# Optimization experiments

Hardware: AMD Instinct MI355X
Metric: run time of the kernel (lower is better)

Reference implementation:

```python
import jax, jax.numpy as jnp
from jax import lax
import numpy as np

B = 512      # instances
C = 64       # cases (segments)
HID = 1024
ATT = 128


def _conv(x, w, b):
    # torch Conv2d(kernel=5, padding=2), NCHW / OIHW layout
    y = lax.conv_general_dilated(x, w, (1, 1), [(2, 2), (2, 2)],
                                 dimension_numbers=('NCHW', 'OIHW', 'NCHW'))
    return y + b[None, :, None, None]


def _pool(x):
    # MaxPool2d(2)
    return lax.reduce_window(x, -jnp.inf, lax.max, (1, 1, 2, 2), (1, 1, 2, 2), 'VALID')


def setup_inputs() -> dict:
    key = jax.random.key(0)
    ks = jax.random.split(key, 20)

    def rn(k, shape, scale=0.05):
        return jax.random.normal(k, shape, dtype=jnp.float32) * scale

    inp = {
        'data': jax.random.normal(ks[0], (B, 3, 128, 128), dtype=jnp.float32),
        'case_ids': jnp.sort(jax.random.randint(ks[1], (B,), 0, C, dtype=jnp.int32)),
    }
    chans = [(3, 8), (8, 16), (16, 32), (32, 64), (64, 128)]
    for i, (ci, co) in enumerate(chans):
        inp[f'conv_w{i + 1}'] = rn(ks[2 + 2 * i], (co, ci, 5, 5))
        inp[f'conv_b{i + 1}'] = jnp.zeros((co,), jnp.float32)
    inp['fc_w'] = rn(ks[12], (HID, 128 * 4 * 4), 0.02)
    inp['fc_b'] = jnp.zeros((HID,), jnp.float32)
    inp['att_w1'] = rn(ks[13], (ATT, HID), 0.02)
    inp['att_b1'] = jnp.zeros((ATT,), jnp.float32)
    inp['att_w2'] = rn(ks[14], (1, ATT), 0.02)
    inp['att_b2'] = jnp.zeros((1,), jnp.float32)
    inp['clf_w'] = rn(ks[15], (1, HID), 0.02)
    inp['clf_b'] = jnp.zeros((1,), jnp.float32)
    return inp


def reference(data, case_ids, conv_w1, conv_b1, conv_w2, conv_b2, conv_w3, conv_b3,
              conv_w4, conv_b4, conv_w5, conv_b5, fc_w, fc_b,
              att_w1, att_b1, att_w2, att_b2, clf_w, clf_b):
    x = data
    for w, b in ((conv_w1, conv_b1), (conv_w2, conv_b2), (conv_w3, conv_b3),
                 (conv_w4, conv_b4), (conv_w5, conv_b5)):
        x = jax.nn.relu(_pool(_conv(x, w, b)))
    emb = x.reshape(x.shape[0], -1) @ fc_w.T + fc_b          # (B, HID)

    # --- segment (per-case) attention pooling, vectorized over all cases ---
    logits = (jnp.tanh(emb @ att_w1.T + att_b1) @ att_w2.T + att_b2)[:, 0]  # (B,)
    seg_max = jax.ops.segment_max(logits, case_ids, num_segments=C)
    seg_max = jnp.where(jnp.isfinite(seg_max), seg_max, 0.0)  # guard empty segments
    e = jnp.exp(logits - lax.stop_gradient(seg_max)[case_ids])
    denom = jax.ops.segment_sum(e, case_ids, num_segments=C)
    wgt = e / denom[case_ids]                                  # segment softmax
    aggr = jax.ops.segment_sum(wgt[:, None] * emb, case_ids, num_segments=C)  # (C, HID)

    # --- classifier ---
    return jax.nn.sigmoid(aggr @ clf_w.T + clf_b)              # (C, 1)
```

## Files before the change

kernel.cpp:

```cpp
#include <hip/hip_runtime.h>
#include <hip/hip_bf16.h>
#include <math.h>

#define BATCH 512
#define NSEG  64
#define HID   1024
#define ATT   128

typedef __attribute__((ext_vector_type(8))) __bf16 bf16x8;
typedef __attribute__((ext_vector_type(4))) __bf16 bf16x4;
typedef __attribute__((ext_vector_type(4))) float  f32x4;

__device__ inline void wcv(const float* __restrict__ w, __bf16* __restrict__ wt,
                           int t, int Ci, int Co) {
    int j  = t & 7;
    int t2 = t >> 3;
    int co = t2 % Co;
    int k8 = t2 / Co;
    int k  = k8 * 8 + j;
    int tap = k / Ci, ci = k % Ci;
    wt[t] = (__bf16)w[(co * Ci + ci) * 25 + tap];
}

__global__ void wprep_k(const float* __restrict__ cw1, const float* __restrict__ cw2,
                        const float* __restrict__ cw3, const float* __restrict__ cw4,
                        const float* __restrict__ cw5, const float* __restrict__ fcw,
                        __bf16* __restrict__ wt1, __bf16* __restrict__ wt2,
                        __bf16* __restrict__ wt3, __bf16* __restrict__ wt4,
                        __bf16* __restrict__ wt5, __bf16* __restrict__ wfc) {
    int t = blockIdx.x * 256 + threadIdx.x;
    if (t < 2048) {
        int j = t & 7, m = (t >> 3) & 15, k8 = t >> 7;
        int k = k8 * 8 + j, tap = k >> 2, ci = k & 3;
        float v = 0.f;
        if (m < 8 && ci < 3 && tap < 25) v = cw1[(m * 3 + ci) * 25 + tap];
        wt1[t] = (__bf16)v;
        return;
    }
    t -= 2048;
    if (t < 3200)  { wcv(cw2, wt2, t, 8, 16);   return; }
    t -= 3200;
    if (t < 12800) { wcv(cw3, wt3, t, 16, 32);  return; }
    t -= 12800;
    if (t < 51200) { wcv(cw4, wt4, t, 32, 64);  return; }
    t -= 51200;
    if (t < 204800){ wcv(cw5, wt5, t, 64, 128); return; }
    t -= 204800;
    if (t < 2097152) {
        int j = t & 7, t2 = t >> 3, o = t2 & 1023, k8 = t2 >> 10;
        wfc[t] = (__bf16)fcw[(size_t)o * 2048 + k8 * 8 + j];
    }
}

__global__ void watt_k(const float* __restrict__ w, __bf16* __restrict__ wt) {
    int t = blockIdx.x * 256 + threadIdx.x;
    if (t >= 131072) return;
    int j  = t & 7;
    int t2 = t >> 3;
    int o  = t2 & 127;
    int k8 = t2 >> 7;
    wt[t] = (__bf16)w[(size_t)o * 1024 + k8 * 8 + j];
}

__global__ __launch_bounds__(256) void conv1_mfma_k(
    const float* __restrict__ in, const __bf16* __restrict__ Wt,
    const float* __restrict__ bias, __bf16* __restrict__ out) {
    constexpr int W  = 128;
    constexpr int R  = 4;
    constexpr int RP = R + 4;
    constexpr int WP = W + 4;

    __shared__ __align__(16) __bf16 xs[RP * WP * 4];

    const int tid = threadIdx.x;
    const int b   = blockIdx.x >> 5;
    const int y0  = (blockIdx.x & 31) * R;
    const float* inb = in + (size_t)b * 3 * 16384;

    if (tid < RP * 4) {
        int r = tid >> 2, s = tid & 3;
        int c = (s < 2) ? s : (128 + s);
        *(bf16x4*)(xs + (r * WP + c) * 4) = (bf16x4){};
    }
    {
        int r  = tid >> 5;
        int g  = tid & 31;
        int gy = y0 + r - 2;
        int c0 = g * 4;
        bf16x8 lo = {}, hi = {};
        if ((unsigned)gy < 128u) {
            const float* p = inb + (size_t)gy * 128 + c0;
            float4 a = *(const float4*)(p);
            float4 q = *(const float4*)(p + 16384);
            float4 c = *(const float4*)(p + 32768);
            lo[0] = (__bf16)a.x; lo[1] = (__bf16)q.x; lo[2] = (__bf16)c.x;
            lo[4] = (__bf16)a.y; lo[5] = (__bf16)q.y; lo[6] = (__bf16)c.y;
            hi[0] = (__bf16)a.z; hi[1] = (__bf16)q.z; hi[2] = (__bf16)c.z;
            hi[4] = (__bf16)a.w; hi[5] = (__bf16)q.w; hi[6] = (__bf16)c.w;
        }
        *(bf16x8*)(xs + (r * WP + c0 + 2) * 4)     = lo;
        *(bf16x8*)(xs + (r * WP + c0 + 2) * 4 + 8) = hi;
    }
    __syncthreads();

    const int lane = tid & 63, wave = tid >> 6;
    const int quad = lane >> 4, l15 = lane & 15;
    constexpr int F = 8;

    int pbase[F];
    f32x4 acc[F];
#pragma unroll
    for (int f = 0; f < F; ++f) {
        int row = 2 * (wave >> 1) + (f >> 2);
        int col = (wave & 1) * 64 + (f & 3) * 16 + l15;
        pbase[f] = ((row + 2) * WP + col + 2) * 8;
        acc[f] = f32x4{0.f, 0.f, 0.f, 0.f};
    }
    const char* xsb = (const char*)xs;

#pragma unroll
    for (int kt = 0; kt < 4; ++kt) {
        int k8 = kt * 4 + quad;
        int tap0 = k8 * 2, tap1 = tap0 + 1;
        int t0 = tap0 < 25 ? tap0 : 0;
        int t1 = tap1 < 25 ? tap1 : 0;
        int s0 = ((t0 / 5 - 2) * WP + (t0 % 5 - 2)) * 8;
        int s1 = ((t1 / 5 - 2) * WP + (t1 % 5 - 2)) * 8;
        bf16x8 av = *(const bf16x8*)(Wt + ((size_t)k8 * 16 + l15) * 8);
#pragma unroll
        for (int f = 0; f < F; ++f) {
            bf16x4 b0 = *(const bf16x4*)(xsb + pbase[f] + s0);
            bf16x4 b1 = *(const bf16x4*)(xsb + pbase[f] + s1);
            bf16x8 bv = __builtin_shufflevector(b0, b1, 0, 1, 2, 3, 4, 5, 6, 7);
            acc[f] = __builtin_amdgcn_mfma_f32_16x16x32_bf16(av, bv, acc[f], 0, 0, 0);
        }
    }

    {
        int cog  = (quad & 1) * 4;
        bool on  = ((l15 & 1) == 0) && (quad < 2);
        int oy   = (y0 >> 1) + (wave >> 1);
        float4 b4 = *(const float4*)(bias + cog);
#pragma unroll
        for (int f = 0; f < 4; ++f) {
            int ox = (wave & 1) * 32 + f * 8 + (l15 >> 1);
            bf16x4 ov;
#pragma unroll
            for (int r = 0; r < 4; ++r) {
                float v0 = acc[f][r], v1 = acc[f + 4][r];
                float h = fmaxf(fmaxf(v0, __shfl_xor(v0, 1)),
                                fmaxf(v1, __shfl_xor(v1, 1)));
                ov[r] = (__bf16)fmaxf(h + ((const float*)&b4)[r], 0.f);
            }
            if (on)
                *(bf16x4*)(out + ((size_t)b * 4096 + oy * 64 + ox) * 8 + cog) = ov;
        }
    }
}

template<int Ci, int Co, int H, int RB, int IMGS, int OUTMODE, int CS>
__global__ __launch_bounds__(256) void conv2d_mfma_k(
    const __bf16* __restrict__ X, const __bf16* __restrict__ Wt,
    const float* __restrict__ bias, void* __restrict__ outp) {
    constexpr int W    = H;
    constexpr int PW   = W + 4;
    constexpr int PR   = RB + 4;
    constexpr int PIX  = RB * W;
    constexpr int P    = IMGS * PIX;
    constexpr int SE   = Ci + (Ci >= 16 ? 8 : 0);
    constexpr int SB   = SE * 2;
    constexpr int K    = 25 * Ci;
    constexpr int KTF  = K / 32;
    constexpr int FW   = P / 64;
    constexpr int NCOT = Co / 16 / CS;
    constexpr int C8   = Ci / 8;
    constexpr int BPI  = H / RB;
    constexpr int OW   = W / 2;

    __shared__ __align__(16) char smem[IMGS * PR * PW * SB];

    const int tid = threadIdx.x;
    const int b0  = (blockIdx.x / BPI) * IMGS;
    const int y0  = (blockIdx.x % BPI) * RB;
    const int co0 = blockIdx.y * (NCOT * 16);

    constexpr int NSLOT = IMGS * PR * PW * C8;
    for (int i = tid; i < NSLOT; i += 256) {
        int s   = i % C8;
        int t2  = i / C8;
        int pc  = t2 % PW;
        int t3  = t2 / PW;
        int pr  = t3 % PR;
        int img = t3 / PR;
        int gy  = y0 + pr - 2;
        int gx  = pc - 2;
        bf16x8 v = {};
        if ((unsigned)gy < (unsigned)H && (unsigned)gx < (unsigned)W)
            v = *(const bf16x8*)(X + (((size_t)(b0 + img) * H + gy) * W + gx) * Ci + s * 8);
        *(bf16x8*)(smem + ((size_t)(img * PR + pr) * PW + pc) * SB + s * 16) = v;
    }
    __syncthreads();

    const int lane = tid & 63, wave = tid >> 6;
    const int quad = lane >> 4, l15 = lane & 15;

    int pbase[FW];
    f32x4 acc[FW][NCOT];
    int rg = 0, ch = 0, gbase = 0, img5 = 0;
    if constexpr (W >= 16) {
        constexpr int C16 = W / 16;
        ch = wave % C16;
        rg = wave / C16;
#pragma unroll
        for (int f = 0; f < FW; ++f) {
            int row = rg * FW + f;
            pbase[f] = ((row + 2) * PW + ch * 16 + l15 + 2) * SB;
        }
    } else {
        img5  = wave >> 1;
        gbase = (wave & 1) * FW;
#pragma unroll
        for (int f = 0; f < FW; ++f) {
            int g    = gbase + f;
            int row0 = 2 * g + (l15 >> 3);
            pbase[f] = ((img5 * PR + row0 + 2) * PW + (l15 & 7) + 2) * SB;
        }
    }
#pragma unroll
    for (int f = 0; f < FW; ++f)
#pragma unroll
        for (int c = 0; c < NCOT; ++c) acc[f][c] = f32x4{0.f, 0.f, 0.f, 0.f};

    const bf16x8 BZ = {};
    auto kstep = [&](int kt, bool mask) {
        int k8 = kt * 4 + quad;
        int kk = k8 * 8;
        bool kok = true;
        if (mask) { kok = kk < K; if (!kok) { k8 = 0; kk = 0; } }
        int tap = kk / Ci, cio = kk % Ci;
        int dy = tap / 5 - 2, dx = tap % 5 - 2;
        int shift = (dy * PW + dx) * SB + cio * 2;
        bf16x8 bv[FW];
#pragma unroll
        for (int f = 0; f < FW; ++f) {
            bv[f] = *(const bf16x8*)(smem + pbase[f] + shift);
            if (mask && !kok) bv[f] = BZ;
        }
#pragma unroll
        for (int c = 0; c < NCOT; ++c) {
            bf16x8 av = *(const bf16x8*)(Wt + ((size_t)k8 * Co + co0 + c * 16 + l15) * 8);
#pragma unroll
            for (int f = 0; f < FW; ++f)
                acc[f][c] = __builtin_amdgcn_mfma_f32_16x16x32_bf16(av, bv[f], acc[f][c], 0, 0, 0);
        }
    };
#pragma unroll 2
    for (int kt = 0; kt < KTF; ++kt) kstep(kt, false);
    if constexpr (K % 32 != 0) kstep(KTF, true);

    if constexpr (W >= 16) {
#pragma unroll
        for (int fp = 0; fp < FW / 2; ++fp) {
            int f0  = 2 * fp;
            int row = rg * FW + f0;
            int oy  = (y0 + row) >> 1;
            int ox  = (ch * 16 + l15) >> 1;
            bool on = (l15 & 1) == 0;
#pragma unroll
            for (int c = 0; c < NCOT; ++c) {
                float4 bb = *(const float4*)(bias + co0 + c * 16 + quad * 4);
                bf16x4 ov;
#pragma unroll
                for (int r = 0; r < 4; ++r) {
                    float v0 = acc[f0][c][r];
                    float h0 = fmaxf(v0, __shfl_xor(v0, 1));
                    float v1 = acc[f0 + 1][c][r];
                    float h1 = fmaxf(v1, __shfl_xor(v1, 1));
                    float m  = fmaxf(h0, h1) + ((const float*)&bb)[r];
                    ov[r] = (__bf16)fmaxf(m, 0.f);
                }
                if (on)
                    *(bf16x4*)((__bf16*)outp +
                        (((size_t)b0 * (H / 2) + oy) * OW + ox) * Co + co0 + c * 16 + quad * 4) = ov;
            }
        }
    } else {
#pragma unroll
        for (int f = 0; f < FW; ++f) {
            int g   = gbase + f;
            bool on = ((l15 & 1) == 0) && (l15 < 8);
            int ox  = (l15 & 7) >> 1;
#pragma unroll
            for (int c = 0; c < NCOT; ++c) {
                float4 bb = *(const float4*)(bias + co0 + c * 16 + quad * 4);
#pragma unroll
                for (int r = 0; r < 4; ++r) {
                    float v  = acc[f][c][r];
                    float h  = fmaxf(v, __shfl_xor(v, 1));
                    float m2 = fmaxf(h, __shfl_xor(h, 8));
                    float m  = fmaxf(m2 + ((const float*)&bb)[r], 0.f);
                    if (on)
                        ((__bf16*)outp)[(size_t)(b0 + img5) * 2048 +
                            (co0 + c * 16 + quad * 4 + r) * 16 + g * 4 + ox] = (__bf16)m;
                }
            }
        }
    }
}

__global__ __launch_bounds__(256) void fc_mfma_k(
    const __bf16* __restrict__ Xb, const __bf16* __restrict__ Wfc,
    const float* __restrict__ bias, float* __restrict__ emb,
    __bf16* __restrict__ embb) {
    const int tid  = threadIdx.x;
    const int lane = tid & 63, wave = tid >> 6;
    const int quad = lane >> 4, l15 = lane & 15;
    const int n0   = blockIdx.x * 128;
    const int co0  = blockIdx.y * 16;

    int n[2];
    f32x4 acc[2];
#pragma unroll
    for (int f = 0; f < 2; ++f) {
        n[f] = n0 + wave * 32 + f * 16 + l15;
        acc[f] = f32x4{0.f, 0.f, 0.f, 0.f};
    }

#pragma unroll 4
    for (int kt = 0; kt < 64; ++kt) {
        int k8 = kt * 4 + quad;
        bf16x8 av = *(const bf16x8*)(Wfc + ((size_t)k8 * 1024 + co0 + l15) * 8);
#pragma unroll
        for (int f = 0; f < 2; ++f) {
            bf16x8 bv = *(const bf16x8*)(Xb + (size_t)n[f] * 2048 + k8 * 8);
            acc[f] = __builtin_amdgcn_mfma_f32_16x16x32_bf16(av, bv, acc[f], 0, 0, 0);
        }
    }

    float4 b4 = *(const float4*)(bias + co0 + quad * 4);
#pragma unroll
    for (int f = 0; f < 2; ++f) {
        f32x4 v = acc[f];
        v[0] += b4.x; v[1] += b4.y; v[2] += b4.z; v[3] += b4.w;
        *(f32x4*)(emb + (size_t)n[f] * 1024 + co0 + quad * 4) = v;
        bf16x4 eb;
        eb[0] = (__bf16)v[0]; eb[1] = (__bf16)v[1];
        eb[2] = (__bf16)v[2]; eb[3] = (__bf16)v[3];
        *(bf16x4*)(embb + (size_t)n[f] * 1024 + co0 + quad * 4) = eb;
    }
}

__global__ __launch_bounds__(256) void att_mfma_k(
    const __bf16* __restrict__ embb, const __bf16* __restrict__ Wa,
    const float* __restrict__ b1, const float* __restrict__ w2,
    const float* __restrict__ b2, float* __restrict__ logits) {
    const int tid = threadIdx.x, lane = tid & 63, wave = tid >> 6;
    const int quad = lane >> 4, l15 = lane & 15;
    const int n = blockIdx.x * 16 + l15;

    f32x4 acc[2];
    acc[0] = f32x4{0.f, 0.f, 0.f, 0.f};
    acc[1] = f32x4{0.f, 0.f, 0.f, 0.f};

#pragma unroll 4
    for (int kt = 0; kt < 32; ++kt) {
        int k8 = kt * 4 + quad;
        bf16x8 bv = *(const bf16x8*)(embb + (size_t)n * 1024 + k8 * 8);
#pragma unroll
        for (int t = 0; t < 2; ++t) {
            int o0 = (wave * 2 + t) * 16;
            bf16x8 av = *(const bf16x8*)(Wa + ((size_t)k8 * 128 + o0 + l15) * 8);
            acc[t] = __builtin_amdgcn_mfma_f32_16x16x32_bf16(av, bv, acc[t], 0, 0, 0);
        }
    }

    float s = 0.f;
#pragma unroll
    for (int t = 0; t < 2; ++t) {
#pragma unroll
        for (int r = 0; r < 4; ++r) {
            int o = (wave * 2 + t) * 16 + quad * 4 + r;
            s += tanhf(acc[t][r] + b1[o]) * w2[o];
        }
    }
    s += __shfl_xor(s, 16);
    s += __shfl_xor(s, 32);

    __shared__ float part[4][16];
    if (lane < 16) part[wave][l15] = s;
    __syncthreads();
    if (tid < 16)
        logits[blockIdx.x * 16 + tid] =
            part[0][tid] + part[1][tid] + part[2][tid] + part[3][tid] + b2[0];
}

__global__ __launch_bounds__(256) void segment_k(
    const float* __restrict__ emb, const float* __restrict__ logits,
    const int* __restrict__ cid, const float* __restrict__ clf_w,
    const float* __restrict__ clf_b, float* __restrict__ out) {
    const int c = blockIdx.x;
    const int t = threadIdx.x;
    __shared__ int cids[BATCH];
    __shared__ float red[256];
    for (int i = t; i < BATCH; i += 256) cids[i] = cid[i];
    __syncthreads();

    float lm = -1e30f;
    for (int b = t; b < BATCH; b += 256)
        if (cids[b] == c) lm = fmaxf(lm, logits[b]);
    red[t] = lm; __syncthreads();
    for (int s = 128; s > 0; s >>= 1) {
        if (t < s) red[t] = fmaxf(red[t], red[t + s]);
        __syncthreads();
    }
    float smax = red[0]; __syncthreads();

    float ls = 0.f;
    for (int b = t; b < BATCH; b += 256)
        if (cids[b] == c) ls += expf(logits[b] - smax);
    red[t] = ls; __syncthreads();
    for (int s = 128; s > 0; s >>= 1) {
        if (t < s) red[t] += red[t + s];
        __syncthreads();
    }
    float denom = red[0]; __syncthreads();
    float inv = (denom > 0.f) ? 1.f / denom : 0.f;

    const int h0 = t * 4;
    float g0 = 0.f, g1 = 0.f, g2 = 0.f, g3 = 0.f;
    for (int b = 0; b < BATCH; ++b) {
        if (cids[b] == c) {
            float wgt = expf(logits[b] - smax) * inv;
            float4 ev = *(const float4*)(emb + (size_t)b * HID + h0);
            g0 = fmaf(wgt, ev.x, g0);
            g1 = fmaf(wgt, ev.y, g1);
            g2 = fmaf(wgt, ev.z, g2);
            g3 = fmaf(wgt, ev.w, g3);
        }
    }
    float4 cw = *(const float4*)(clf_w + h0);
    float ca = g0 * cw.x + g1 * cw.y + g2 * cw.z + g3 * cw.w;
    red[t] = ca; __syncthreads();
    for (int s = 128; s > 0; s >>= 1) {
        if (t < s) red[t] += red[t + s];
        __syncthreads();
    }
    if (t == 0) out[c] = 1.f / (1.f + expf(-(red[0] + clf_b[0])));
}

extern "C" void kernel_launch(void* const* d_in, const int* in_sizes, int n_in,
                              void* d_out, int out_size, void* d_ws, size_t ws_size,
                              hipStream_t stream) {
    const float* data = (const float*)d_in[0];
    const int*   cid  = (const int*)d_in[1];
    const float* cw1 = (const float*)d_in[2],  * cb1 = (const float*)d_in[3];
    const float* cw2 = (const float*)d_in[4],  * cb2 = (const float*)d_in[5];
    const float* cw3 = (const float*)d_in[6],  * cb3 = (const float*)d_in[7];
    const float* cw4 = (const float*)d_in[8],  * cb4 = (const float*)d_in[9];
    const float* cw5 = (const float*)d_in[10], * cb5 = (const float*)d_in[11];
    const float* fcw = (const float*)d_in[12], * fcb = (const float*)d_in[13];
    const float* aw1 = (const float*)d_in[14], * ab1 = (const float*)d_in[15];
    const float* aw2 = (const float*)d_in[16], * ab2 = (const float*)d_in[17];
    const float* clw = (const float*)d_in[18], * clb = (const float*)d_in[19];
    float* out = (float*)d_out;

    char* wsb = (char*)d_ws;
    __bf16* x1  = (__bf16*)(wsb);
    __bf16* x2  = (__bf16*)(wsb + 33554432);
    __bf16* x3  = (__bf16*)(wsb + 50331648);
    __bf16* x4  = (__bf16*)(wsb + 58720256);
    __bf16* x5b = (__bf16*)(wsb + 62914560);
    float*  emb = (float*) (wsb + 65011712);
    float*  lg  = (float*) (wsb + 67108864);
    __bf16* wt2 = (__bf16*)(wsb + 67110912);
    __bf16* wt3 = (__bf16*)(wsb + 67117312);
    __bf16* wt4 = (__bf16*)(wsb + 67142912);
    __bf16* wt5 = (__bf16*)(wsb + 67245312);
    __bf16* wfc = (__bf16*)(wsb + 67654912);
    __bf16* wt1 = (__bf16*)(wsb + 71849216);
    __bf16* wa   = (__bf16*)(wsb);
    __bf16* embb = (__bf16*)(wsb + 1048576);

    wprep_k<<<9263, 256, 0, stream>>>(cw1, cw2, cw3, cw4, cw5, fcw,
                                      wt1, wt2, wt3, wt4, wt5, wfc);

    conv1_mfma_k<<<16384, 256, 0, stream>>>(data, wt1, cb1, x1);

    conv2d_mfma_k<8,  16,  64, 8, 1, 0, 1><<<4096, 256, 0, stream>>>(x1, wt2, cb2, x2);
    watt_k<<<512, 256, 0, stream>>>(aw1, wa);
    conv2d_mfma_k<16, 32,  32, 8, 1, 0, 1><<<2048, 256, 0, stream>>>(x2, wt3, cb3, x3);
    conv2d_mfma_k<32, 64,  16, 8, 1, 0, 1><<<1024, 256, 0, stream>>>(x3, wt4, cb4, x4);
    conv2d_mfma_k<64, 128, 8,  8, 2, 1, 2><<<dim3(256, 2), 256, 0, stream>>>(x4, wt5, cb5, x5b);

    fc_mfma_k<<<dim3(4, 64), 256, 0, stream>>>(x5b, wfc, fcb, emb, embb);
    att_mfma_k<<<32, 256, 0, stream>>>(embb, wa, ab1, aw2, ab2, lg);
    segment_k<<<NSEG, 256, 0, stream>>>(emb, lg, cid, clw, clb, out);
}
```

Before: 426.4 us.

## Enlarge conv1 row tile with LDS-staged pooling epilogue; split conv4 and fc work

conv1 now processes 8 rows per block instead of 4. The input halo is amortized over more rows, and the 2x2 maxpool epilogue goes through a shared-memory staging buffer rather than lane shuffles, so every thread stores coalesced output. conv4 splits its output channels across two grid slices, and the fc kernel gives each wave a single 16-row tile on twice as many blocks. The aim is to cut redundant halo loads and raise parallelism in the small late layers, at the cost of extra LDS traffic, two more barriers and higher register use in conv1.

```diff
diff --git a/kernel.cpp b/kernel.cpp
--- a/kernel.cpp
+++ b/kernel.cpp
@@ -66,15 +66,20 @@
     const float* __restrict__ in, const __bf16* __restrict__ Wt,
     const float* __restrict__ bias, __bf16* __restrict__ out) {
     constexpr int W  = 128;
-    constexpr int R  = 4;
+    constexpr int R  = 8;
     constexpr int RP = R + 4;
     constexpr int WP = W + 4;
-
-    __shared__ __align__(16) __bf16 xs[RP * WP * 4];
+    constexpr int CSTR = R * W + 4;
+    constexpr int XS_B = RP * WP * 4 * 2;
+    constexpr int CS_B = 8 * CSTR * 4;
+
+    __shared__ __align__(16) char smem[CS_B > XS_B ? CS_B : XS_B];
+    __bf16* xs = (__bf16*)smem;
+    float*  cs = (float*)smem;
 
     const int tid = threadIdx.x;
-    const int b   = blockIdx.x >> 5;
-    const int y0  = (blockIdx.x & 31) * R;
+    const int b   = blockIdx.x >> 4;
+    const int y0  = (blockIdx.x & 15) * R;
     const float* inb = in + (size_t)b * 3 * 16384;
 
     if (tid < RP * 4) {
@@ -82,9 +87,9 @@
         int c = (s < 2) ? s : (128 + s);
         *(bf16x4*)(xs + (r * WP + c) * 4) = (bf16x4){};
     }
-    {
-        int r  = tid >> 5;
-        int g  = tid & 31;
+    for (int i = tid; i < RP * 32; i += 256) {
+        int r  = i >> 5;
+        int g  = i & 31;
         int gy = y0 + r - 2;
         int c0 = g * 4;
         bf16x8 lo = {}, hi = {};
@@ -105,18 +110,13 @@
 
     const int lane = tid & 63, wave = tid >> 6;
     const int quad = lane >> 4, l15 = lane & 15;
-    constexpr int F = 8;
-
-    int pbase[F];
+    constexpr int F = 16;
+
+    const int cbase = (((wave * 2) + 2) * WP + l15 + 2) * 8;
     f32x4 acc[F];
 #pragma unroll
-    for (int f = 0; f < F; ++f) {
-        int row = 2 * (wave >> 1) + (f >> 2);
-        int col = (wave & 1) * 64 + (f & 3) * 16 + l15;
-        pbase[f] = ((row + 2) * WP + col + 2) * 8;
-        acc[f] = f32x4{0.f, 0.f, 0.f, 0.f};
-    }
-    const char* xsb = (const char*)xs;
+    for (int f = 0; f < F; ++f) acc[f] = f32x4{0.f, 0.f, 0.f, 0.f};
+    const char* xsb = (const char*)smem;
 
 #pragma unroll
     for (int kt = 0; kt < 4; ++kt) {
@@ -129,32 +129,44 @@
         bf16x8 av = *(const bf16x8*)(Wt + ((size_t)k8 * 16 + l15) * 8);
 #pragma unroll
         for (int f = 0; f < F; ++f) {
-            bf16x4 b0 = *(const bf16x4*)(xsb + pbase[f] + s0);
-            bf16x4 b1 = *(const bf16x4*)(xsb + pbase[f] + s1);
+            int pb = cbase + (f >> 3) * (WP * 8) + (f & 7) * 128;
+            bf16x4 b0 = *(const bf16x4*)(xsb + pb + s0);
+            bf16x4 b1 = *(const bf16x4*)(xsb + pb + s1);
             bf16x8 bv = __builtin_shufflevector(b0, b1, 0, 1, 2, 3, 4, 5, 6, 7);
             acc[f] = __builtin_amdgcn_mfma_f32_16x16x32_bf16(av, bv, acc[f], 0, 0, 0);
         }
     }
 
-    {
-        int cog  = (quad & 1) * 4;
-        bool on  = ((l15 & 1) == 0) && (quad < 2);
-        int oy   = (y0 >> 1) + (wave >> 1);
+    __syncthreads();
+#pragma unroll
+    for (int f = 0; f < F; ++f) {
+        int pl = (wave * 2 + (f >> 3)) * 128 + (f & 7) * 16 + l15;
+#pragma unroll
+        for (int r = 0; r < 4; ++r) {
+            int m = quad * 4 + r;
+            if (m < 8) cs[m * CSTR + pl] = acc[f][r];
+        }
+    }
+    __syncthreads();
+
+#pragma unroll
+    for (int it = 0; it < 2; ++it) {
+        int oi  = (tid >> 1) + it * 128;
+        int cog = (tid & 1) * 4;
+        int oyl = oi >> 6, ox = oi & 63;
+        int pl0 = oyl * 2 * 128 + ox * 2;
         float4 b4 = *(const float4*)(bias + cog);
-#pragma unroll
-        for (int f = 0; f < 4; ++f) {
-            int ox = (wave & 1) * 32 + f * 8 + (l15 >> 1);
-            bf16x4 ov;
-#pragma unroll
-            for (int r = 0; r < 4; ++r) {
-                float v0 = acc[f][r], v1 = acc[f + 4][r];
-                float h = fmaxf(fmaxf(v0, __shfl_xor(v0, 1)),
-                                fmaxf(v1, __shfl_xor(v1, 1)));
-                ov[r] = (__bf16)fmaxf(h + ((const float*)&b4)[r], 0.f);
-            }
-            if (on)
-                *(bf16x4*)(out + ((size_t)b * 4096 + oy * 64 + ox) * 8 + cog) = ov;
-        }
+        bf16x4 ov;
+#pragma unroll
+        for (int i = 0; i < 4; ++i) {
+            int cr = cog + i;
+            float v0 = cs[cr * CSTR + pl0],       v1 = cs[cr * CSTR + pl0 + 1];
+            float v2 = cs[cr * CSTR + pl0 + 128], v3 = cs[cr * CSTR + pl0 + 129];
+            float m = fmaxf(fmaxf(v0, v1), fmaxf(v2, v3)) + ((const float*)&b4)[i];
+            ov[i] = (__bf16)fmaxf(m, 0.f);
+        }
+        size_t ob = ((size_t)b * 4096 + (size_t)((y0 >> 1) + oyl) * 64 + ox) * 8 + cog;
+        *(bf16x4*)(out + ob) = ov;
     }
 }
 
@@ -315,39 +327,27 @@
     const int tid  = threadIdx.x;
     const int lane = tid & 63, wave = tid >> 6;
     const int quad = lane >> 4, l15 = lane & 15;
-    const int n0   = blockIdx.x * 128;
+    const int n    = blockIdx.x * 64 + wave * 16 + l15;
     const int co0  = blockIdx.y * 16;
 
-    int n[2];
-    f32x4 acc[2];
-#pragma unroll
-    for (int f = 0; f < 2; ++f) {
-        n[f] = n0 + wave * 32 + f * 16 + l15;
-        acc[f] = f32x4{0.f, 0.f, 0.f, 0.f};
-    }
-
-#pragma unroll 4
+    f32x4 acc = f32x4{0.f, 0.f, 0.f, 0.f};
+
+#pragma unroll 8
     for (int kt = 0; kt < 64; ++kt) {
         int k8 = kt * 4 + quad;
         bf16x8 av = *(const bf16x8*)(Wfc + ((size_t)k8 * 1024 + co0 + l15) * 8);
-#pragma unroll
-        for (int f = 0; f < 2; ++f) {
-            bf16x8 bv = *(const bf16x8*)(Xb + (size_t)n[f] * 2048 + k8 * 8);
-            acc[f] = __builtin_amdgcn_mfma_f32_16x16x32_bf16(av, bv, acc[f], 0, 0, 0);
-        }
+        bf16x8 bv = *(const bf16x8*)(Xb + (size_t)n * 2048 + k8 * 8);
+        acc = __builtin_amdgcn_mfma_f32_16x16x32_bf16(av, bv, acc, 0, 0, 0);
     }
 
     float4 b4 = *(const float4*)(bias + co0 + quad * 4);
-#pragma unroll
-    for (int f = 0; f < 2; ++f) {
-        f32x4 v = acc[f];
-        v[0] += b4.x; v[1] += b4.y; v[2] += b4.z; v[3] += b4.w;
-        *(f32x4*)(emb + (size_t)n[f] * 1024 + co0 + quad * 4) = v;
-        bf16x4 eb;
-        eb[0] = (__bf16)v[0]; eb[1] = (__bf16)v[1];
-        eb[2] = (__bf16)v[2]; eb[3] = (__bf16)v[3];
-        *(bf16x4*)(embb + (size_t)n[f] * 1024 + co0 + quad * 4) = eb;
-    }
+    f32x4 v = acc;
+    v[0] += b4.x; v[1] += b4.y; v[2] += b4.z; v[3] += b4.w;
+    *(f32x4*)(emb + (size_t)n * 1024 + co0 + quad * 4) = v;
+    bf16x4 eb;
+    eb[0] = (__bf16)v[0]; eb[1] = (__bf16)v[1];
+    eb[2] = (__bf16)v[2]; eb[3] = (__bf16)v[3];
+    *(bf16x4*)(embb + (size_t)n * 1024 + co0 + quad * 4) = eb;
 }
 
 __global__ __launch_bounds__(256) void att_mfma_k(
@@ -484,15 +484,15 @@
     wprep_k<<<9263, 256, 0, stream>>>(cw1, cw2, cw3, cw4, cw5, fcw,
                                       wt1, wt2, wt3, wt4, wt5, wfc);
 
-    conv1_mfma_k<<<16384, 256, 0, stream>>>(data, wt1, cb1, x1);
+    conv1_mfma_k<<<8192, 256, 0, stream>>>(data, wt1, cb1, x1);
 
     conv2d_mfma_k<8,  16,  64, 8, 1, 0, 1><<<4096, 256, 0, stream>>>(x1, wt2, cb2, x2);
     watt_k<<<512, 256, 0, stream>>>(aw1, wa);
     conv2d_mfma_k<16, 32,  32, 8, 1, 0, 1><<<2048, 256, 0, stream>>>(x2, wt3, cb3, x3);
-    conv2d_mfma_k<32, 64,  16, 8, 1, 0, 1><<<1024, 256, 0, stream>>>(x3, wt4, cb4, x4);
+    conv2d_mfma_k<32, 64,  16, 8, 1, 0, 2><<<dim3(1024, 2), 256, 0, stream>>>(x3, wt4, cb4, x4);
     conv2d_mfma_k<64, 128, 8,  8, 2, 1, 2><<<dim3(256, 2), 256, 0, stream>>>(x4, wt5, cb5, x5b);
 
-    fc_mfma_k<<<dim3(4, 64), 256, 0, stream>>>(x5b, wfc, fcb, emb, embb);
+    fc_mfma_k<<<dim3(8, 64), 256, 0, stream>>>(x5b, wfc, fcb, emb, embb);
     att_mfma_k<<<32, 256, 0, stream>>>(embb, wa, ab1, aw2, ab2, lg);
     segment_k<<<NSEG, 256, 0, stream>>>(emb, lg, cid, clw, clb, out);
 }
```

Result: faster. 411.2 us (-3.6%).
